# Optimization experiments

Hardware: AMD Instinct MI355X
Metric: run time of the kernel (lower is better)

## Reference

```python
import jax, jax.numpy as jnp
import numpy as np

N = 262144
DIM = 256
NUM_HEADS = 4
HEAD_DIM = DIM // NUM_HEADS
B = 4096
SCALE = HEAD_DIM ** (-0.5)
EPS = 1e-8


def setup_inputs() -> dict:
    key = jax.random.key(0)
    ks = jax.random.split(key, 7)
    x = jax.random.normal(ks[0], (N, DIM), dtype=jnp.float32)
    batch = jnp.sort(jax.random.randint(ks[1], (N,), 0, B)).astype(jnp.int64)
    query = jax.random.normal(ks[2], (NUM_HEADS, HEAD_DIM), dtype=jnp.float32)
    # nn.Linear default init scale ~ 1/sqrt(dim); keep exp() well-behaved
    key_w = jax.random.normal(ks[3], (DIM, DIM), dtype=jnp.float32) / np.sqrt(DIM)
    key_b = jax.random.normal(ks[4], (DIM,), dtype=jnp.float32) * 0.01
    value_w = jax.random.normal(ks[5], (DIM, DIM), dtype=jnp.float32) / np.sqrt(DIM)
    value_b = jax.random.normal(ks[6], (DIM,), dtype=jnp.float32) * 0.01
    return {"x": x, "batch": batch, "query": query, "key_w": key_w,
            "key_b": key_b, "value_w": value_w, "value_b": value_b}


def reference(x, batch, query, key_w, key_b, value_w, value_b):
    # k, v: [N, H, Hd]  (torch Linear: x @ W.T + b)
    k = (x @ key_w.T + key_b).reshape(N, NUM_HEADS, HEAD_DIM)
    v = (x @ value_w.T + value_b).reshape(N, NUM_HEADS, HEAD_DIM)
    # attn: [N, H] -- dot of learned per-head query with each node's key
    attn = jnp.einsum('hd,nhd->nh', query, k) * SCALE
    attn_exp = jnp.exp(attn)  # faithful: no max-subtraction in original
    # segment softmax denominator gathered back to nodes: [N, H]
    attn_sum = jax.ops.segment_sum(attn_exp, batch, num_segments=B)[batch]
    attn_norm = attn_exp / (attn_sum + EPS)
    # weighted values scatter-added per segment: [B, H, Hd]
    weighted = attn_norm[:, :, None] * v
    pooled = jax.ops.segment_sum(weighted, batch, num_segments=B)
    return pooled.reshape(B, DIM)
```

## Files before the change

kernel.cpp:

```cpp
#include <hip/hip_runtime.h>


constexpr int DIM = 256;
constexpr int NH  = 4;
constexpr int HD  = 64;
constexpr float SCL  = 0.125f;
constexpr float EPSV = 1e-8f;

constexpr int WS_QW   = 0;
constexpr int WS_QB   = 1024;
constexpr int WS_OFFS = 1088;
constexpr int WS_VWT  = 8192;
constexpr int WS_SRAW = 73728;

__global__ void prep_qw(const float* __restrict__ query,
                        const float* __restrict__ key_w,
                        const float* __restrict__ key_b,
                        float* __restrict__ ws){
  int t = blockIdx.x * 256 + threadIdx.x;
  int h = t >> 8, j = t & 255;
  float acc = 0.f;
  #pragma unroll 8
  for (int d = 0; d < HD; ++d)
    acc += query[h*HD+d] * key_w[(size_t)(h*HD+d)*DIM + j];
  ws[WS_QW + t] = acc;
  if (j == 0){
    float bb = 0.f;
    for (int d = 0; d < HD; ++d)
      bb += query[h*HD+d] * key_b[h*HD+d];
    ws[WS_QB + h] = bb;
  }
}

__global__ void prep_vwt(const float* __restrict__ value_w, float* __restrict__ ws){
  int jj = blockIdx.x;
  int t  = threadIdx.x;
  float4 v = *(const float4*)(value_w + (size_t)t*DIM + 4*jj);
  ((float4*)(ws + WS_VWT))[jj*256 + t] = v;
}

__global__ void seg_offsets(const int* __restrict__ batch32,
                            int* __restrict__ offs, int N, int B){
  int i = blockIdx.x * 256 + threadIdx.x;
  if (i >= N) return;
  const bool is64 = (batch32[N-1] == 0);
  int v  = is64 ? batch32[2*i] : batch32[i];
  int vp = (i == 0) ? -1 : (is64 ? batch32[2*(i-1)] : batch32[i-1]);
  for (int b = vp + 1; b <= v; ++b) offs[b] = i;
  if (i == N-1)
    for (int b = v + 1; b <= B; ++b) offs[b] = N;
}

__global__ __launch_bounds__(256, 4)
void attn_pool_split(const float* __restrict__ x,
                     const int* __restrict__ offs,
                     const float* __restrict__ ws,
                     float* __restrict__ sraw,
                     float* __restrict__ esum){
  __shared__ __align__(16) float S_all[4][NH*DIM];
  __shared__ float sums_all[4][NH];

  const int bid = blockIdx.x;
  const int b   = bid >> 1, part = bid & 1;
  const int tid = threadIdx.x;
  const int s = offs[b], e = offs[b+1];
  const int len = e - s;
  const int h1  = (len + 1) >> 1;
  const int ps  = s + part * h1;
  const int pe  = part ? e : (s + h1);

  const int wave = tid >> 6, lane = tid & 63;
  const int half = lane >> 5, sl = lane & 31;
  const int sigma = wave * 2 + half;

  float qwr[NH][8];
  #pragma unroll
  for (int h = 0; h < NH; ++h){
    float4 a = *(const float4*)(ws + WS_QW + h*DIM + 4*sl);
    float4 c = *(const float4*)(ws + WS_QW + h*DIM + 128 + 4*sl);
    qwr[h][0]=a.x; qwr[h][1]=a.y; qwr[h][2]=a.z; qwr[h][3]=a.w;
    qwr[h][4]=c.x; qwr[h][5]=c.y; qwr[h][6]=c.z; qwr[h][7]=c.w;
  }
  float qb[NH];
  #pragma unroll
  for (int h = 0; h < NH; ++h) qb[h] = ws[WS_QB + h];

  float Sacc[NH][8];
  #pragma unroll
  for (int h = 0; h < NH; ++h)
    #pragma unroll
    for (int c = 0; c < 8; ++c) Sacc[h][c] = 0.f;
  float se[NH] = {0.f, 0.f, 0.f, 0.f};

  const float4* xr4 = (const float4*)x;
  const float4 Z = make_float4(0.f, 0.f, 0.f, 0.f);

  int n0 = ps + sigma*2;
  bool v0 = n0 < pe;
  bool v1 = n0 + 1 < pe;
  float4 a0=Z, b0=Z, a1=Z, b1=Z;
  if (v0){ a0 = xr4[(size_t)n0*64 + sl];     b0 = xr4[(size_t)n0*64 + 32 + sl]; }
  if (v1){ a1 = xr4[(size_t)(n0+1)*64 + sl]; b1 = xr4[(size_t)(n0+1)*64 + 32 + sl]; }

  while (v0){
    const int nn = n0 + 16;
    const bool w0 = nn < pe;
    const bool w1 = nn + 1 < pe;
    float4 c0=Z, d0=Z, c1=Z, d1=Z;
    if (w0){ c0 = xr4[(size_t)nn*64 + sl];     d0 = xr4[(size_t)nn*64 + 32 + sl]; }
    if (w1){ c1 = xr4[(size_t)(nn+1)*64 + sl]; d1 = xr4[(size_t)(nn+1)*64 + 32 + sl]; }

    float xv0[8] = {a0.x,a0.y,a0.z,a0.w,b0.x,b0.y,b0.z,b0.w};
    float xv1[8] = {a1.x,a1.y,a1.z,a1.w,b1.x,b1.y,b1.z,b1.w};

    float p0[NH], p1[NH];
    #pragma unroll
    for (int h = 0; h < NH; ++h){
      float s0 = 0.f, s1 = 0.f;
      #pragma unroll
      for (int c = 0; c < 8; ++c){ s0 += qwr[h][c]*xv0[c]; s1 += qwr[h][c]*xv1[c]; }
      p0[h] = s0; p1[h] = s1;
    }
    #pragma unroll
    for (int m = 1; m < 32; m <<= 1){
      #pragma unroll
      for (int h = 0; h < NH; ++h){
        p0[h] += __shfl_xor(p0[h], m, 64);
        p1[h] += __shfl_xor(p1[h], m, 64);
      }
    }
    const float g1 = v1 ? 1.f : 0.f;
    #pragma unroll
    for (int h = 0; h < NH; ++h){
      float e0 = __expf((p0[h] + qb[h]) * SCL);
      float e1 = __expf((p1[h] + qb[h]) * SCL) * g1;
      se[h] += e0 + e1;
      #pragma unroll
      for (int c = 0; c < 8; ++c)
        Sacc[h][c] += e0*xv0[c] + e1*xv1[c];
    }
    n0 = nn; v0 = w0; v1 = w1;
    a0 = c0; b0 = d0; a1 = c1; b1 = d1;
  }

  #pragma unroll
  for (int h = 0; h < NH; ++h){
    se[h] += __shfl_xor(se[h], 32, 64);
    #pragma unroll
    for (int c = 0; c < 8; ++c) Sacc[h][c] += __shfl_xor(Sacc[h][c], 32, 64);
  }
  if (half == 0){
    #pragma unroll
    for (int h = 0; h < NH; ++h){
      float4 lo = make_float4(Sacc[h][0], Sacc[h][1], Sacc[h][2], Sacc[h][3]);
      float4 hi = make_float4(Sacc[h][4], Sacc[h][5], Sacc[h][6], Sacc[h][7]);
      *(float4*)&S_all[wave][h*DIM + 4*sl]       = lo;
      *(float4*)&S_all[wave][h*DIM + 128 + 4*sl] = hi;
    }
    if (sl == 0){
      #pragma unroll
      for (int h = 0; h < NH; ++h) sums_all[wave][h] = se[h];
    }
  }
  __syncthreads();

  #pragma unroll
  for (int k = 0; k < 4; ++k){
    const int idx = tid + k*256;
    float sv = 0.f;
    #pragma unroll
    for (int w = 0; w < 4; ++w) sv += S_all[w][idx];
    sraw[(size_t)bid*1024 + idx] = sv;
  }
  if (tid < NH){
    float tot = 0.f;
    #pragma unroll
    for (int w = 0; w < 4; ++w) tot += sums_all[w][tid];
    esum[bid*4 + tid] = tot;
  }
}

__global__ __launch_bounds__(256, 4)
void val_proj(const float* __restrict__ ws,
              const float* __restrict__ sraw,
              const float* __restrict__ esum,
              const float* __restrict__ value_b,
              float* __restrict__ out){
  constexpr int TB = 8;
  __shared__ __align__(16) float Sl[NH*DIM*TB];
  const int b0  = blockIdx.x * TB;
  const int tid = threadIdx.x;

  for (int idx = tid; idx < NH*DIM*TB; idx += 256){
    const int i = idx >> 10, rem = idx & 1023;
    const size_t base = (size_t)(b0 + i) * 2048;
    Sl[rem*TB + i] = sraw[base + rem] + sraw[base + 1024 + rem];
  }
  __syncthreads();

  const int t = tid, h = t >> 6;
  const float4* vwt4 = (const float4*)(ws + WS_VWT);
  float acc[TB];
  #pragma unroll
  for (int i = 0; i < TB; ++i) acc[i] = 0.f;

  #pragma unroll 4
  for (int jj = 0; jj < 64; ++jj){
    const float4 w4 = vwt4[jj*256 + t];
    #pragma unroll
    for (int r = 0; r < 4; ++r){
      const float* sp = &Sl[(h*256 + 4*jj + r)*TB];
      const float4 s0 = *(const float4*)sp;
      const float4 s1 = *(const float4*)(sp + 4);
      const float wr = (&w4.x)[r];
      acc[0] += wr*s0.x; acc[1] += wr*s0.y; acc[2] += wr*s0.z; acc[3] += wr*s0.w;
      acc[4] += wr*s1.x; acc[5] += wr*s1.y; acc[6] += wr*s1.z; acc[7] += wr*s1.w;
    }
  }
  const float vb = value_b[t];
  #pragma unroll
  for (int i = 0; i < TB; ++i){
    const float es  = esum[(b0 + i)*8 + h] + esum[(b0 + i)*8 + 4 + h];
    const float inv = 1.f / (es + EPSV);
    out[(size_t)(b0 + i)*256 + t] = acc[i]*inv + es*inv*vb;
  }
}

template<int MODE>
__global__ __launch_bounds__(512, 4)
void attn_pool_fused(const float* __restrict__ x,
                     const int* __restrict__ offs,
                     const float* __restrict__ ws,
                     const float* __restrict__ value_w,
                     const float* __restrict__ value_b,
                     float* __restrict__ out){
  constexpr int LDSF = (MODE == 1) ? (8192 + 32 + 1024 + 2048 + 8)
                                   : (8192 + 32 + 1024 + 512 + 8);
  __shared__ __align__(16) float lds[LDSF];
  float* S_all    = lds;
  float* sums_all = lds + 8192;

  const int b   = blockIdx.x;
  const int tid = threadIdx.x;
  const int seg_start = offs[b];
  const int seg_end   = offs[b+1];

  const int wave = tid >> 6, lane = tid & 63;
  const int half = lane >> 5, sl = lane & 31;
  const int sigma = wave * 2 + half;

  float qwr[NH][8];
  #pragma unroll
  for (int h = 0; h < NH; ++h){
    float4 a = *(const float4*)(ws + WS_QW + h*DIM + 4*sl);
    float4 c = *(const float4*)(ws + WS_QW + h*DIM + 128 + 4*sl);
    qwr[h][0]=a.x; qwr[h][1]=a.y; qwr[h][2]=a.z; qwr[h][3]=a.w;
    qwr[h][4]=c.x; qwr[h][5]=c.y; qwr[h][6]=c.z; qwr[h][7]=c.w;
  }
  float qb[NH];
  #pragma unroll
  for (int h = 0; h < NH; ++h) qb[h] = ws[WS_QB + h];

  float Sacc[NH][8];
  #pragma unroll
  for (int h = 0; h < NH; ++h)
    #pragma unroll
    for (int c = 0; c < 8; ++c) Sacc[h][c] = 0.f;
  float se[NH] = {0.f, 0.f, 0.f, 0.f};

  const float4* xr4 = (const float4*)x;
  const float4 Z = make_float4(0.f, 0.f, 0.f, 0.f);

  int n0 = seg_start + sigma*2;
  bool v0 = n0 < seg_end;
  bool v1 = n0 + 1 < seg_end;
  float4 a0=Z, b0=Z, a1=Z, b1=Z;
  if (v0){ a0 = xr4[(size_t)n0*64 + sl];     b0 = xr4[(size_t)n0*64 + 32 + sl]; }
  if (v1){ a1 = xr4[(size_t)(n0+1)*64 + sl]; b1 = xr4[(size_t)(n0+1)*64 + 32 + sl]; }

  while (v0){
    const int nn = n0 + 32;
    const bool w0 = nn < seg_end;
    const bool w1 = nn + 1 < seg_end;
    float4 c0=Z, d0=Z, c1=Z, d1=Z;
    if (w0){ c0 = xr4[(size_t)nn*64 + sl];     d0 = xr4[(size_t)nn*64 + 32 + sl]; }
    if (w1){ c1 = xr4[(size_t)(nn+1)*64 + sl]; d1 = xr4[(size_t)(nn+1)*64 + 32 + sl]; }

    float xv0[8] = {a0.x,a0.y,a0.z,a0.w,b0.x,b0.y,b0.z,b0.w};
    float xv1[8] = {a1.x,a1.y,a1.z,a1.w,b1.x,b1.y,b1.z,b1.w};

    float p0[NH], p1[NH];
    #pragma unroll
    for (int h = 0; h < NH; ++h){
      float s0 = 0.f, s1 = 0.f;
      #pragma unroll
      for (int c = 0; c < 8; ++c){ s0 += qwr[h][c]*xv0[c]; s1 += qwr[h][c]*xv1[c]; }
      p0[h] = s0; p1[h] = s1;
    }
    #pragma unroll
    for (int m = 1; m < 32; m <<= 1){
      #pragma unroll
      for (int h = 0; h < NH; ++h){
        p0[h] += __shfl_xor(p0[h], m, 64);
        p1[h] += __shfl_xor(p1[h], m, 64);
      }
    }
    const float g1 = v1 ? 1.f : 0.f;
    #pragma unroll
    for (int h = 0; h < NH; ++h){
      float e0 = __expf((p0[h] + qb[h]) * SCL);
      float e1 = __expf((p1[h] + qb[h]) * SCL) * g1;
      se[h] += e0 + e1;
      #pragma unroll
      for (int c = 0; c < 8; ++c)
        Sacc[h][c] += e0*xv0[c] + e1*xv1[c];
    }
    n0 = nn; v0 = w0; v1 = w1;
    a0 = c0; b0 = d0; a1 = c1; b1 = d1;
  }

  #pragma unroll
  for (int h = 0; h < NH; ++h){
    se[h] += __shfl_xor(se[h], 32, 64);
    #pragma unroll
    for (int c = 0; c < 8; ++c) Sacc[h][c] += __shfl_xor(Sacc[h][c], 32, 64);
  }
  if (half == 0){
    #pragma unroll
    for (int h = 0; h < NH; ++h){
      float4 lo = make_float4(Sacc[h][0], Sacc[h][1], Sacc[h][2], Sacc[h][3]);
      float4 hi = make_float4(Sacc[h][4], Sacc[h][5], Sacc[h][6], Sacc[h][7]);
      *(float4*)&S_all[wave*1024 + h*DIM + 4*sl]       = lo;
      *(float4*)&S_all[wave*1024 + h*DIM + 128 + 4*sl] = hi;
    }
    if (sl == 0){
      #pragma unroll
      for (int h = 0; h < NH; ++h) sums_all[wave*4 + h] = se[h];
    }
  }
  __syncthreads();

  float* Sfin  = lds + 8224;
  float* invs  = (MODE == 1) ? lds + 11296 : lds + 9760;
  float* wsums = invs + 4;
  #pragma unroll
  for (int k = 0; k < 2; ++k){
    const int idx = tid + k*512;
    float sv = 0.f;
    #pragma unroll
    for (int w = 0; w < 8; ++w) sv += S_all[w*1024 + idx];
    Sfin[idx] = sv;
  }
  if (tid < NH){
    float tot = 0.f;
    #pragma unroll
    for (int w = 0; w < 8; ++w) tot += sums_all[w*4 + tid];
    float inv = 1.f / (tot + EPSV);
    invs[tid] = inv; wsums[tid] = tot * inv;
  }
  __syncthreads();

  if constexpr (MODE == 1){
    float* ep = lds + 9248;
    const float4* vwt4 = (const float4*)(ws + WS_VWT);
    const int hh = lane >> 4;
    float4 acc = make_float4(0.f, 0.f, 0.f, 0.f);
    for (int jj = wave*8; jj < wave*8 + 8; ++jj){
      float4 q0 = vwt4[jj*256 + 4*lane + 0];
      float4 q1 = vwt4[jj*256 + 4*lane + 1];
      float4 q2 = vwt4[jj*256 + 4*lane + 2];
      float4 q3 = vwt4[jj*256 + 4*lane + 3];
      float4 sf = *(const float4*)&Sfin[hh*256 + 4*jj];
      acc.x += q0.x*sf.x + q0.y*sf.y + q0.z*sf.z + q0.w*sf.w;
      acc.y += q1.x*sf.x + q1.y*sf.y + q1.z*sf.z + q1.w*sf.w;
      acc.z += q2.x*sf.x + q2.y*sf.y + q2.z*sf.z + q2.w*sf.w;
      acc.w += q3.x*sf.x + q3.y*sf.y + q3.z*sf.z + q3.w*sf.w;
    }
    *(float4*)&ep[wave*256 + 4*lane] = acc;
    __syncthreads();
    if (tid < 256){
      const int t = tid, h2 = t >> 6;
      float sv = 0.f;
      #pragma unroll
      for (int w = 0; w < 8; ++w) sv += ep[w*256 + t];
      out[(size_t)b*256 + t] = sv * invs[h2] + wsums[h2] * value_b[t];
    }
  } else {
    float* ep2 = lds + 9248;
    const int t = tid & 255, part = tid >> 8;
    const int h2 = t >> 6;
    const float4* vrow = (const float4*)(value_w + (size_t)t * DIM) + part*32;
    const float4* sp   = (const float4*)&Sfin[h2*256] + part*32;
    float acc = 0.f;
    #pragma unroll
    for (int q = 0; q < 32; ++q){
      float4 r = vrow[q];
      float4 sv = sp[q];
      acc += r.x*sv.x + r.y*sv.y + r.z*sv.z + r.w*sv.w;
    }
    ep2[part*256 + t] = acc;
    __syncthreads();
    if (part == 0)
      out[(size_t)b * DIM + t] = (ep2[t] + ep2[256 + t]) * invs[h2] + wsums[h2] * value_b[t];
  }
}

extern "C" void kernel_launch(void* const* d_in, const int* in_sizes, int n_in,
                              void* d_out, int out_size, void* d_ws, size_t ws_size,
                              hipStream_t stream){
  const float* x       = (const float*)d_in[0];
  const int*   batch   = (const int*)d_in[1];
  const float* query   = (const float*)d_in[2];
  const float* key_w   = (const float*)d_in[3];
  const float* key_b   = (const float*)d_in[4];
  const float* value_w = (const float*)d_in[5];
  const float* value_b = (const float*)d_in[6];
  float* ws  = (float*)d_ws;
  float* out = (float*)d_out;

  const int N = in_sizes[1];
  const int B = out_size / DIM;

  int*   offs = (int*)(ws + WS_OFFS);
  float* sraw = ws + WS_SRAW;
  float* esum = ws + WS_SRAW + (size_t)B*2048;

  const size_t need_split = ((size_t)WS_SRAW + (size_t)B*2048 + (size_t)B*8) * sizeof(float);
  const size_t need_vwt   = ((size_t)WS_VWT + 65536) * sizeof(float);

  prep_qw<<<4, 256, 0, stream>>>(query, key_w, key_b, ws);
  seg_offsets<<<(N + 255) / 256, 256, 0, stream>>>(batch, offs, N, B);

  if (ws_size >= need_split){
    prep_vwt<<<64, 256, 0, stream>>>(value_w, ws);
    attn_pool_split<<<2*B, 256, 0, stream>>>(x, offs, ws, sraw, esum);
    val_proj<<<B / 8, 256, 0, stream>>>(ws, sraw, esum, value_b, out);
  } else if (ws_size >= need_vwt){
    prep_vwt<<<64, 256, 0, stream>>>(value_w, ws);
    attn_pool_fused<1><<<B, 512, 0, stream>>>(x, offs, ws, value_w, value_b, out);
  } else {
    attn_pool_fused<2><<<B, 512, 0, stream>>>(x, offs, ws, value_w, value_b, out);
  }
}
```

Before: 410.5 us.

## Use one block per segment with full-wave rows and padded LDS in projection

The attention pooling kernel now runs one block per segment instead of two half-segment blocks. Each wave covers a whole 256-float row per node (one float4 per lane) and processes four nodes per iteration with a full 64-lane reduction. This removes the second partial-sum buffer and the cross-block combine in the projection kernel, and halves the sraw traffic. The projection kernel pads its shared layout to stride 9, trading vector LDS loads for scalar loads to avoid bank conflicts. The cost is half as many blocks, so less parallelism on uneven segments, and more shuffle steps per node.

```diff
diff --git a/kernel.cpp b/kernel.cpp
--- a/kernel.cpp
+++ b/kernel.cpp
@@ -52,131 +52,112 @@
 }
 
 __global__ __launch_bounds__(256, 4)
-void attn_pool_split(const float* __restrict__ x,
-                     const int* __restrict__ offs,
-                     const float* __restrict__ ws,
-                     float* __restrict__ sraw,
-                     float* __restrict__ esum){
+void attn_pool3(const float* __restrict__ x,
+                const int* __restrict__ offs,
+                const float* __restrict__ ws,
+                float* __restrict__ sraw,
+                float* __restrict__ esum){
   __shared__ __align__(16) float S_all[4][NH*DIM];
   __shared__ float sums_all[4][NH];
 
-  const int bid = blockIdx.x;
-  const int b   = bid >> 1, part = bid & 1;
+  const int b   = blockIdx.x;
   const int tid = threadIdx.x;
   const int s = offs[b], e = offs[b+1];
-  const int len = e - s;
-  const int h1  = (len + 1) >> 1;
-  const int ps  = s + part * h1;
-  const int pe  = part ? e : (s + h1);
 
   const int wave = tid >> 6, lane = tid & 63;
-  const int half = lane >> 5, sl = lane & 31;
-  const int sigma = wave * 2 + half;
-
-  float qwr[NH][8];
+
+  float qwr[NH][4];
   #pragma unroll
   for (int h = 0; h < NH; ++h){
-    float4 a = *(const float4*)(ws + WS_QW + h*DIM + 4*sl);
-    float4 c = *(const float4*)(ws + WS_QW + h*DIM + 128 + 4*sl);
-    qwr[h][0]=a.x; qwr[h][1]=a.y; qwr[h][2]=a.z; qwr[h][3]=a.w;
-    qwr[h][4]=c.x; qwr[h][5]=c.y; qwr[h][6]=c.z; qwr[h][7]=c.w;
+    float4 q = *(const float4*)(ws + WS_QW + h*DIM + 4*lane);
+    qwr[h][0]=q.x; qwr[h][1]=q.y; qwr[h][2]=q.z; qwr[h][3]=q.w;
   }
   float qb[NH];
   #pragma unroll
   for (int h = 0; h < NH; ++h) qb[h] = ws[WS_QB + h];
 
-  float Sacc[NH][8];
+  float Sacc[NH][4];
   #pragma unroll
   for (int h = 0; h < NH; ++h)
     #pragma unroll
-    for (int c = 0; c < 8; ++c) Sacc[h][c] = 0.f;
+    for (int c = 0; c < 4; ++c) Sacc[h][c] = 0.f;
   float se[NH] = {0.f, 0.f, 0.f, 0.f};
 
   const float4* xr4 = (const float4*)x;
-  const float4 Z = make_float4(0.f, 0.f, 0.f, 0.f);
-
-  int n0 = ps + sigma*2;
-  bool v0 = n0 < pe;
-  bool v1 = n0 + 1 < pe;
-  float4 a0=Z, b0=Z, a1=Z, b1=Z;
-  if (v0){ a0 = xr4[(size_t)n0*64 + sl];     b0 = xr4[(size_t)n0*64 + 32 + sl]; }
-  if (v1){ a1 = xr4[(size_t)(n0+1)*64 + sl]; b1 = xr4[(size_t)(n0+1)*64 + 32 + sl]; }
-
-  while (v0){
+
+  int n0 = s + (wave << 2);
+  float4 A[4]; bool g[4];
+  #pragma unroll
+  for (int i = 0; i < 4; ++i){
+    g[i] = (n0 + i) < e;
+    const int safe = g[i] ? (n0 + i) : 0;
+    A[i] = xr4[(size_t)safe * 64 + lane];
+  }
+
+  while (n0 < e){
     const int nn = n0 + 16;
-    const bool w0 = nn < pe;
-    const bool w1 = nn + 1 < pe;
-    float4 c0=Z, d0=Z, c1=Z, d1=Z;
-    if (w0){ c0 = xr4[(size_t)nn*64 + sl];     d0 = xr4[(size_t)nn*64 + 32 + sl]; }
-    if (w1){ c1 = xr4[(size_t)(nn+1)*64 + sl]; d1 = xr4[(size_t)(nn+1)*64 + 32 + sl]; }
-
-    float xv0[8] = {a0.x,a0.y,a0.z,a0.w,b0.x,b0.y,b0.z,b0.w};
-    float xv1[8] = {a1.x,a1.y,a1.z,a1.w,b1.x,b1.y,b1.z,b1.w};
-
-    float p0[NH], p1[NH];
-    #pragma unroll
-    for (int h = 0; h < NH; ++h){
-      float s0 = 0.f, s1 = 0.f;
-      #pragma unroll
-      for (int c = 0; c < 8; ++c){ s0 += qwr[h][c]*xv0[c]; s1 += qwr[h][c]*xv1[c]; }
-      p0[h] = s0; p1[h] = s1;
-    }
-    #pragma unroll
-    for (int m = 1; m < 32; m <<= 1){
+    float4 An[4]; bool gn[4];
+    #pragma unroll
+    for (int i = 0; i < 4; ++i){
+      gn[i] = (nn + i) < e;
+      const int safe = gn[i] ? (nn + i) : 0;
+      An[i] = xr4[(size_t)safe * 64 + lane];
+    }
+
+    float p[4][NH];
+    #pragma unroll
+    for (int i = 0; i < 4; ++i)
+      #pragma unroll
+      for (int h = 0; h < NH; ++h)
+        p[i][h] = qwr[h][0]*A[i].x + qwr[h][1]*A[i].y
+                + qwr[h][2]*A[i].z + qwr[h][3]*A[i].w;
+
+    #pragma unroll
+    for (int m = 1; m < 64; m <<= 1){
+      #pragma unroll
+      for (int i = 0; i < 4; ++i)
+        #pragma unroll
+        for (int h = 0; h < NH; ++h)
+          p[i][h] += __shfl_xor(p[i][h], m, 64);
+    }
+
+    #pragma unroll
+    for (int i = 0; i < 4; ++i){
       #pragma unroll
       for (int h = 0; h < NH; ++h){
-        p0[h] += __shfl_xor(p0[h], m, 64);
-        p1[h] += __shfl_xor(p1[h], m, 64);
+        const float ev = g[i] ? __expf((p[i][h] + qb[h]) * SCL) : 0.f;
+        se[h] += ev;
+        Sacc[h][0] += ev * A[i].x;
+        Sacc[h][1] += ev * A[i].y;
+        Sacc[h][2] += ev * A[i].z;
+        Sacc[h][3] += ev * A[i].w;
       }
     }
-    const float g1 = v1 ? 1.f : 0.f;
-    #pragma unroll
-    for (int h = 0; h < NH; ++h){
-      float e0 = __expf((p0[h] + qb[h]) * SCL);
-      float e1 = __expf((p1[h] + qb[h]) * SCL) * g1;
-      se[h] += e0 + e1;
-      #pragma unroll
-      for (int c = 0; c < 8; ++c)
-        Sacc[h][c] += e0*xv0[c] + e1*xv1[c];
-    }
-    n0 = nn; v0 = w0; v1 = w1;
-    a0 = c0; b0 = d0; a1 = c1; b1 = d1;
-  }
-
-  #pragma unroll
-  for (int h = 0; h < NH; ++h){
-    se[h] += __shfl_xor(se[h], 32, 64);
-    #pragma unroll
-    for (int c = 0; c < 8; ++c) Sacc[h][c] += __shfl_xor(Sacc[h][c], 32, 64);
-  }
-  if (half == 0){
-    #pragma unroll
-    for (int h = 0; h < NH; ++h){
-      float4 lo = make_float4(Sacc[h][0], Sacc[h][1], Sacc[h][2], Sacc[h][3]);
-      float4 hi = make_float4(Sacc[h][4], Sacc[h][5], Sacc[h][6], Sacc[h][7]);
-      *(float4*)&S_all[wave][h*DIM + 4*sl]       = lo;
-      *(float4*)&S_all[wave][h*DIM + 128 + 4*sl] = hi;
-    }
-    if (sl == 0){
-      #pragma unroll
-      for (int h = 0; h < NH; ++h) sums_all[wave][h] = se[h];
-    }
+
+    n0 = nn;
+    #pragma unroll
+    for (int i = 0; i < 4; ++i){ A[i] = An[i]; g[i] = gn[i]; }
+  }
+
+  #pragma unroll
+  for (int h = 0; h < NH; ++h)
+    *(float4*)&S_all[wave][h*DIM + 4*lane] =
+        make_float4(Sacc[h][0], Sacc[h][1], Sacc[h][2], Sacc[h][3]);
+  if (lane == 0){
+    #pragma unroll
+    for (int h = 0; h < NH; ++h) sums_all[wave][h] = se[h];
   }
   __syncthreads();
 
   #pragma unroll
   for (int k = 0; k < 4; ++k){
     const int idx = tid + k*256;
-    float sv = 0.f;
-    #pragma unroll
-    for (int w = 0; w < 4; ++w) sv += S_all[w][idx];
-    sraw[(size_t)bid*1024 + idx] = sv;
+    const float sv = S_all[0][idx] + S_all[1][idx] + S_all[2][idx] + S_all[3][idx];
+    sraw[(size_t)b*1024 + idx] = sv;
   }
   if (tid < NH){
-    float tot = 0.f;
-    #pragma unroll
-    for (int w = 0; w < 4; ++w) tot += sums_all[w][tid];
-    esum[bid*4 + tid] = tot;
+    esum[b*4 + tid] = sums_all[0][tid] + sums_all[1][tid]
+                    + sums_all[2][tid] + sums_all[3][tid];
   }
 }
 
@@ -186,15 +167,15 @@
               const float* __restrict__ esum,
               const float* __restrict__ value_b,
               float* __restrict__ out){
-  constexpr int TB = 8;
-  __shared__ __align__(16) float Sl[NH*DIM*TB];
+  constexpr int TB  = 8;
+  constexpr int TBP = 9;
+  __shared__ __align__(16) float Sl[NH*DIM*TBP];
   const int b0  = blockIdx.x * TB;
   const int tid = threadIdx.x;
 
   for (int idx = tid; idx < NH*DIM*TB; idx += 256){
     const int i = idx >> 10, rem = idx & 1023;
-    const size_t base = (size_t)(b0 + i) * 2048;
-    Sl[rem*TB + i] = sraw[base + rem] + sraw[base + 1024 + rem];
+    Sl[rem*TBP + i] = sraw[(size_t)(b0 + i)*1024 + rem];
   }
   __syncthreads();
 
@@ -209,18 +190,16 @@
     const float4 w4 = vwt4[jj*256 + t];
     #pragma unroll
     for (int r = 0; r < 4; ++r){
-      const float* sp = &Sl[(h*256 + 4*jj + r)*TB];
-      const float4 s0 = *(const float4*)sp;
-      const float4 s1 = *(const float4*)(sp + 4);
+      const float* sp = &Sl[(h*256 + 4*jj + r)*TBP];
       const float wr = (&w4.x)[r];
-      acc[0] += wr*s0.x; acc[1] += wr*s0.y; acc[2] += wr*s0.z; acc[3] += wr*s0.w;
-      acc[4] += wr*s1.x; acc[5] += wr*s1.y; acc[6] += wr*s1.z; acc[7] += wr*s1.w;
+      acc[0] += wr*sp[0]; acc[1] += wr*sp[1]; acc[2] += wr*sp[2]; acc[3] += wr*sp[3];
+      acc[4] += wr*sp[4]; acc[5] += wr*sp[5]; acc[6] += wr*sp[6]; acc[7] += wr*sp[7];
     }
   }
   const float vb = value_b[t];
   #pragma unroll
   for (int i = 0; i < TB; ++i){
-    const float es  = esum[(b0 + i)*8 + h] + esum[(b0 + i)*8 + 4 + h];
+    const float es  = esum[(b0 + i)*4 + h];
     const float inv = 1.f / (es + EPSV);
     out[(size_t)(b0 + i)*256 + t] = acc[i]*inv + es*inv*vb;
   }
@@ -269,7 +248,7 @@
   float se[NH] = {0.f, 0.f, 0.f, 0.f};
 
   const float4* xr4 = (const float4*)x;
-  const float4 Z = make_float4(0.f, 0.f, 0.f, 0.f);
+  const float4 Z = make_float4(0.f,0.f,0.f,0.f);
 
   int n0 = seg_start + sigma*2;
   bool v0 = n0 < seg_end;
@@ -423,9 +402,9 @@
 
   int*   offs = (int*)(ws + WS_OFFS);
   float* sraw = ws + WS_SRAW;
-  float* esum = ws + WS_SRAW + (size_t)B*2048;
-
-  const size_t need_split = ((size_t)WS_SRAW + (size_t)B*2048 + (size_t)B*8) * sizeof(float);
+  float* esum = ws + WS_SRAW + (size_t)B*1024;
+
+  const size_t need_split = ((size_t)WS_SRAW + (size_t)B*1024 + (size_t)B*4) * sizeof(float);
   const size_t need_vwt   = ((size_t)WS_VWT + 65536) * sizeof(float);
 
   prep_qw<<<4, 256, 0, stream>>>(query, key_w, key_b, ws);
@@ -433,7 +412,7 @@
 
   if (ws_size >= need_split){
     prep_vwt<<<64, 256, 0, stream>>>(value_w, ws);
-    attn_pool_split<<<2*B, 256, 0, stream>>>(x, offs, ws, sraw, esum);
+    attn_pool3<<<B, 256, 0, stream>>>(x, offs, ws, sraw, esum);
     val_proj<<<B / 8, 256, 0, stream>>>(ws, sraw, esum, value_b, out);
   } else if (ws_size >= need_vwt){
     prep_vwt<<<64, 256, 0, stream>>>(value_w, ws);
```

Result: no change. 418.0 us (+1.8%).

## Fuse segment pooling with value projection, merge prep kernels, use DPP reductions

Applied to the files above, without the earlier changes.

Merges the three preparation kernels (query-key fold, value weight transpose, segment offsets) into one launch. It replaces the split-segment pooling plus separate value projection kernel with a single per-segment kernel that reduces in LDS and applies the value projection directly, removing the intermediate sraw/esum round trip through global memory and one launch. The per-row dot-product reduction now uses DPP row rotates plus a ds_swizzle instead of shfl_xor. In exchange each segment is handled by one 256-thread block instead of two, which halves parallelism on the streaming phase, and value_w rows are re-read per segment instead of being reused across 8 segments.

```diff
diff --git a/kernel.cpp b/kernel.cpp
--- a/kernel.cpp
+++ b/kernel.cpp
@@ -11,63 +11,75 @@
 constexpr int WS_QB   = 1024;
 constexpr int WS_OFFS = 1088;
 constexpr int WS_VWT  = 8192;
-constexpr int WS_SRAW = 73728;
-
-__global__ void prep_qw(const float* __restrict__ query,
-                        const float* __restrict__ key_w,
-                        const float* __restrict__ key_b,
-                        float* __restrict__ ws){
-  int t = blockIdx.x * 256 + threadIdx.x;
-  int h = t >> 8, j = t & 255;
-  float acc = 0.f;
-  #pragma unroll 8
-  for (int d = 0; d < HD; ++d)
-    acc += query[h*HD+d] * key_w[(size_t)(h*HD+d)*DIM + j];
-  ws[WS_QW + t] = acc;
-  if (j == 0){
-    float bb = 0.f;
+
+template<int CTRL>
+__device__ __forceinline__ float dpp_ror_add(float v){
+  int r = __builtin_amdgcn_update_dpp(0, __float_as_int(v), CTRL, 0xF, 0xF, false);
+  return v + __int_as_float(r);
+}
+__device__ __forceinline__ float red32(float v){
+  v = dpp_ror_add<0x121>(v);
+  v = dpp_ror_add<0x122>(v);
+  v = dpp_ror_add<0x124>(v);
+  v = dpp_ror_add<0x128>(v);
+  int r = __builtin_amdgcn_ds_swizzle(__float_as_int(v), 0x401F);
+  return v + __int_as_float(r);
+}
+
+__global__ void prep_seg(const float* __restrict__ query,
+                         const float* __restrict__ key_w,
+                         const float* __restrict__ key_b,
+                         const float* __restrict__ value_w,
+                         const int* __restrict__ batch32,
+                         float* __restrict__ ws,
+                         int* __restrict__ offs,
+                         int N, int B, int do_vwt){
+  const int bid = blockIdx.x, tid = threadIdx.x;
+  if (bid < 64){
+    if (do_vwt){
+      float4 v = *(const float4*)(value_w + (size_t)tid*DIM + 4*bid);
+      ((float4*)(ws + WS_VWT))[bid*256 + tid] = v;
+    }
+  } else if (bid < 68){
+    int t = (bid - 64)*256 + tid;
+    int h = t >> 8, j = t & 255;
+    float acc = 0.f;
+    #pragma unroll 8
     for (int d = 0; d < HD; ++d)
-      bb += query[h*HD+d] * key_b[h*HD+d];
-    ws[WS_QB + h] = bb;
-  }
-}
-
-__global__ void prep_vwt(const float* __restrict__ value_w, float* __restrict__ ws){
-  int jj = blockIdx.x;
-  int t  = threadIdx.x;
-  float4 v = *(const float4*)(value_w + (size_t)t*DIM + 4*jj);
-  ((float4*)(ws + WS_VWT))[jj*256 + t] = v;
-}
-
-__global__ void seg_offsets(const int* __restrict__ batch32,
-                            int* __restrict__ offs, int N, int B){
-  int i = blockIdx.x * 256 + threadIdx.x;
-  if (i >= N) return;
-  const bool is64 = (batch32[N-1] == 0);
-  int v  = is64 ? batch32[2*i] : batch32[i];
-  int vp = (i == 0) ? -1 : (is64 ? batch32[2*(i-1)] : batch32[i-1]);
-  for (int b = vp + 1; b <= v; ++b) offs[b] = i;
-  if (i == N-1)
-    for (int b = v + 1; b <= B; ++b) offs[b] = N;
+      acc += query[h*HD+d] * key_w[(size_t)(h*HD+d)*DIM + j];
+    ws[WS_QW + t] = acc;
+    if (j == 0){
+      float bb = 0.f;
+      for (int d = 0; d < HD; ++d)
+        bb += query[h*HD+d] * key_b[h*HD+d];
+      ws[WS_QB + h] = bb;
+    }
+  } else {
+    int i = (bid - 68)*256 + tid;
+    if (i >= N) return;
+    const bool is64 = (batch32[N-1] == 0);
+    int v  = is64 ? batch32[2*i] : batch32[i];
+    int vp = (i == 0) ? -1 : (is64 ? batch32[2*(i-1)] : batch32[i-1]);
+    for (int b = vp + 1; b <= v; ++b) offs[b] = i;
+    if (i == N-1)
+      for (int b = v + 1; b <= B; ++b) offs[b] = N;
+  }
 }
 
 __global__ __launch_bounds__(256, 4)
-void attn_pool_split(const float* __restrict__ x,
-                     const int* __restrict__ offs,
-                     const float* __restrict__ ws,
-                     float* __restrict__ sraw,
-                     float* __restrict__ esum){
+void attn_fused2(const float* __restrict__ x,
+                 const int* __restrict__ offs,
+                 const float* __restrict__ ws,
+                 const float* __restrict__ value_b,
+                 float* __restrict__ out){
   __shared__ __align__(16) float S_all[4][NH*DIM];
+  __shared__ __align__(16) float Sfin[NH*DIM];
   __shared__ float sums_all[4][NH];
-
-  const int bid = blockIdx.x;
-  const int b   = bid >> 1, part = bid & 1;
+  __shared__ float invs[NH], wsums[NH];
+
+  const int b   = blockIdx.x;
   const int tid = threadIdx.x;
   const int s = offs[b], e = offs[b+1];
-  const int len = e - s;
-  const int h1  = (len + 1) >> 1;
-  const int ps  = s + part * h1;
-  const int pe  = part ? e : (s + h1);
 
   const int wave = tid >> 6, lane = tid & 63;
   const int half = lane >> 5, sl = lane & 31;
@@ -95,17 +107,17 @@
   const float4* xr4 = (const float4*)x;
   const float4 Z = make_float4(0.f, 0.f, 0.f, 0.f);
 
-  int n0 = ps + sigma*2;
-  bool v0 = n0 < pe;
-  bool v1 = n0 + 1 < pe;
+  int n0 = s + sigma*2;
+  bool v0 = n0 < e;
+  bool v1 = n0 + 1 < e;
   float4 a0=Z, b0=Z, a1=Z, b1=Z;
   if (v0){ a0 = xr4[(size_t)n0*64 + sl];     b0 = xr4[(size_t)n0*64 + 32 + sl]; }
   if (v1){ a1 = xr4[(size_t)(n0+1)*64 + sl]; b1 = xr4[(size_t)(n0+1)*64 + 32 + sl]; }
 
   while (v0){
     const int nn = n0 + 16;
-    const bool w0 = nn < pe;
-    const bool w1 = nn + 1 < pe;
+    const bool w0 = nn < e;
+    const bool w1 = nn + 1 < e;
     float4 c0=Z, d0=Z, c1=Z, d1=Z;
     if (w0){ c0 = xr4[(size_t)nn*64 + sl];     d0 = xr4[(size_t)nn*64 + 32 + sl]; }
     if (w1){ c1 = xr4[(size_t)(nn+1)*64 + sl]; d1 = xr4[(size_t)(nn+1)*64 + 32 + sl]; }
@@ -122,12 +134,9 @@
       p0[h] = s0; p1[h] = s1;
     }
     #pragma unroll
-    for (int m = 1; m < 32; m <<= 1){
-      #pragma unroll
-      for (int h = 0; h < NH; ++h){
-        p0[h] += __shfl_xor(p0[h], m, 64);
-        p1[h] += __shfl_xor(p1[h], m, 64);
-      }
+    for (int h = 0; h < NH; ++h){
+      p0[h] = red32(p0[h]);
+      p1[h] = red32(p1[h]);
     }
     const float g1 = v1 ? 1.f : 0.f;
     #pragma unroll
@@ -167,66 +176,30 @@
   #pragma unroll
   for (int k = 0; k < 4; ++k){
     const int idx = tid + k*256;
-    float sv = 0.f;
-    #pragma unroll
-    for (int w = 0; w < 4; ++w) sv += S_all[w][idx];
-    sraw[(size_t)bid*1024 + idx] = sv;
+    Sfin[idx] = S_all[0][idx] + S_all[1][idx] + S_all[2][idx] + S_all[3][idx];
   }
   if (tid < NH){
-    float tot = 0.f;
-    #pragma unroll
-    for (int w = 0; w < 4; ++w) tot += sums_all[w][tid];
-    esum[bid*4 + tid] = tot;
-  }
-}
-
-__global__ __launch_bounds__(256, 4)
-void val_proj(const float* __restrict__ ws,
-              const float* __restrict__ sraw,
-              const float* __restrict__ esum,
-              const float* __restrict__ value_b,
-              float* __restrict__ out){
-  constexpr int TB = 8;
-  __shared__ __align__(16) float Sl[NH*DIM*TB];
-  const int b0  = blockIdx.x * TB;
-  const int tid = threadIdx.x;
-
-  for (int idx = tid; idx < NH*DIM*TB; idx += 256){
-    const int i = idx >> 10, rem = idx & 1023;
-    const size_t base = (size_t)(b0 + i) * 2048;
-    Sl[rem*TB + i] = sraw[base + rem] + sraw[base + 1024 + rem];
+    float tot = sums_all[0][tid] + sums_all[1][tid]
+              + sums_all[2][tid] + sums_all[3][tid];
+    float inv = 1.f / (tot + EPSV);
+    invs[tid]  = inv;
+    wsums[tid] = tot * inv;
   }
   __syncthreads();
 
   const int t = tid, h = t >> 6;
   const float4* vwt4 = (const float4*)(ws + WS_VWT);
-  float acc[TB];
-  #pragma unroll
-  for (int i = 0; i < TB; ++i) acc[i] = 0.f;
-
-  #pragma unroll 4
+  const float4* sp   = (const float4*)&Sfin[h*256];
+  float acc = 0.f;
+  #pragma unroll 8
   for (int jj = 0; jj < 64; ++jj){
     const float4 w4 = vwt4[jj*256 + t];
-    #pragma unroll
-    for (int r = 0; r < 4; ++r){
-      const float* sp = &Sl[(h*256 + 4*jj + r)*TB];
-      const float4 s0 = *(const float4*)sp;
-      const float4 s1 = *(const float4*)(sp + 4);
-      const float wr = (&w4.x)[r];
-      acc[0] += wr*s0.x; acc[1] += wr*s0.y; acc[2] += wr*s0.z; acc[3] += wr*s0.w;
-      acc[4] += wr*s1.x; acc[5] += wr*s1.y; acc[6] += wr*s1.z; acc[7] += wr*s1.w;
-    }
-  }
-  const float vb = value_b[t];
-  #pragma unroll
-  for (int i = 0; i < TB; ++i){
-    const float es  = esum[(b0 + i)*8 + h] + esum[(b0 + i)*8 + 4 + h];
-    const float inv = 1.f / (es + EPSV);
-    out[(size_t)(b0 + i)*256 + t] = acc[i]*inv + es*inv*vb;
-  }
-}
-
-template<int MODE>
+    const float4 s4 = sp[jj];
+    acc += w4.x*s4.x + w4.y*s4.y + w4.z*s4.z + w4.w*s4.w;
+  }
+  out[(size_t)b*256 + t] = acc * invs[h] + wsums[h] * value_b[t];
+}
+
 __global__ __launch_bounds__(512, 4)
 void attn_pool_fused(const float* __restrict__ x,
                      const int* __restrict__ offs,
@@ -234,9 +207,7 @@
                      const float* __restrict__ value_w,
                      const float* __restrict__ value_b,
                      float* __restrict__ out){
-  constexpr int LDSF = (MODE == 1) ? (8192 + 32 + 1024 + 2048 + 8)
-                                   : (8192 + 32 + 1024 + 512 + 8);
-  __shared__ __align__(16) float lds[LDSF];
+  __shared__ __align__(16) float lds[8192 + 32 + 1024 + 512 + 8];
   float* S_all    = lds;
   float* sums_all = lds + 8192;
 
@@ -269,7 +240,7 @@
   float se[NH] = {0.f, 0.f, 0.f, 0.f};
 
   const float4* xr4 = (const float4*)x;
-  const float4 Z = make_float4(0.f, 0.f, 0.f, 0.f);
+  const float4 Z = make_float4(0.f,0.f,0.f,0.f);
 
   int n0 = seg_start + sigma*2;
   bool v0 = n0 < seg_end;
@@ -341,7 +312,7 @@
   __syncthreads();
 
   float* Sfin  = lds + 8224;
-  float* invs  = (MODE == 1) ? lds + 11296 : lds + 9760;
+  float* invs  = lds + 9760;
   float* wsums = invs + 4;
   #pragma unroll
   for (int k = 0; k < 2; ++k){
@@ -360,49 +331,22 @@
   }
   __syncthreads();
 
-  if constexpr (MODE == 1){
-    float* ep = lds + 9248;
-    const float4* vwt4 = (const float4*)(ws + WS_VWT);
-    const int hh = lane >> 4;
-    float4 acc = make_float4(0.f, 0.f, 0.f, 0.f);
-    for (int jj = wave*8; jj < wave*8 + 8; ++jj){
-      float4 q0 = vwt4[jj*256 + 4*lane + 0];
-      float4 q1 = vwt4[jj*256 + 4*lane + 1];
-      float4 q2 = vwt4[jj*256 + 4*lane + 2];
-      float4 q3 = vwt4[jj*256 + 4*lane + 3];
-      float4 sf = *(const float4*)&Sfin[hh*256 + 4*jj];
-      acc.x += q0.x*sf.x + q0.y*sf.y + q0.z*sf.z + q0.w*sf.w;
-      acc.y += q1.x*sf.x + q1.y*sf.y + q1.z*sf.z + q1.w*sf.w;
-      acc.z += q2.x*sf.x + q2.y*sf.y + q2.z*sf.z + q2.w*sf.w;
-      acc.w += q3.x*sf.x + q3.y*sf.y + q3.z*sf.z + q3.w*sf.w;
-    }
-    *(float4*)&ep[wave*256 + 4*lane] = acc;
-    __syncthreads();
-    if (tid < 256){
-      const int t = tid, h2 = t >> 6;
-      float sv = 0.f;
-      #pragma unroll
-      for (int w = 0; w < 8; ++w) sv += ep[w*256 + t];
-      out[(size_t)b*256 + t] = sv * invs[h2] + wsums[h2] * value_b[t];
-    }
-  } else {
-    float* ep2 = lds + 9248;
-    const int t = tid & 255, part = tid >> 8;
-    const int h2 = t >> 6;
-    const float4* vrow = (const float4*)(value_w + (size_t)t * DIM) + part*32;
-    const float4* sp   = (const float4*)&Sfin[h2*256] + part*32;
-    float acc = 0.f;
-    #pragma unroll
-    for (int q = 0; q < 32; ++q){
-      float4 r = vrow[q];
-      float4 sv = sp[q];
-      acc += r.x*sv.x + r.y*sv.y + r.z*sv.z + r.w*sv.w;
-    }
-    ep2[part*256 + t] = acc;
-    __syncthreads();
-    if (part == 0)
-      out[(size_t)b * DIM + t] = (ep2[t] + ep2[256 + t]) * invs[h2] + wsums[h2] * value_b[t];
-  }
+  float* ep2 = lds + 9248;
+  const int t = tid & 255, part = tid >> 8;
+  const int h2 = t >> 6;
+  const float4* vrow = (const float4*)(value_w + (size_t)t * DIM) + part*32;
+  const float4* sp   = (const float4*)&Sfin[h2*256] + part*32;
+  float acc = 0.f;
+  #pragma unroll
+  for (int q = 0; q < 32; ++q){
+    float4 r = vrow[q];
+    float4 sv = sp[q];
+    acc += r.x*sv.x + r.y*sv.y + r.z*sv.z + r.w*sv.w;
+  }
+  ep2[part*256 + t] = acc;
+  __syncthreads();
+  if (part == 0)
+    out[(size_t)b * DIM + t] = (ep2[t] + ep2[256 + t]) * invs[h2] + wsums[h2] * value_b[t];
 }
 
 extern "C" void kernel_launch(void* const* d_in, const int* in_sizes, int n_in,
@@ -421,24 +365,16 @@
   const int N = in_sizes[1];
   const int B = out_size / DIM;
 
-  int*   offs = (int*)(ws + WS_OFFS);
-  float* sraw = ws + WS_SRAW;
-  float* esum = ws + WS_SRAW + (size_t)B*2048;
-
-  const size_t need_split = ((size_t)WS_SRAW + (size_t)B*2048 + (size_t)B*8) * sizeof(float);
-  const size_t need_vwt   = ((size_t)WS_VWT + 65536) * sizeof(float);
-
-  prep_qw<<<4, 256, 0, stream>>>(query, key_w, key_b, ws);
-  seg_offsets<<<(N + 255) / 256, 256, 0, stream>>>(batch, offs, N, B);
-
-  if (ws_size >= need_split){
-    prep_vwt<<<64, 256, 0, stream>>>(value_w, ws);
-    attn_pool_split<<<2*B, 256, 0, stream>>>(x, offs, ws, sraw, esum);
-    val_proj<<<B / 8, 256, 0, stream>>>(ws, sraw, esum, value_b, out);
-  } else if (ws_size >= need_vwt){
-    prep_vwt<<<64, 256, 0, stream>>>(value_w, ws);
-    attn_pool_fused<1><<<B, 512, 0, stream>>>(x, offs, ws, value_w, value_b, out);
-  } else {
-    attn_pool_fused<2><<<B, 512, 0, stream>>>(x, offs, ws, value_w, value_b, out);
-  }
-}
+  int* offs = (int*)(ws + WS_OFFS);
+
+  const size_t need_vwt = ((size_t)WS_VWT + 65536) * sizeof(float);
+  const int do_vwt = (ws_size >= need_vwt) ? 1 : 0;
+
+  const int seg_blocks = (N + 255) / 256;
+  prep_seg<<<68 + seg_blocks, 256, 0, stream>>>(query, key_w, key_b, value_w,
+                                                batch, ws, offs, N, B, do_vwt);
+  if (do_vwt)
+    attn_fused2<<<B, 256, 0, stream>>>(x, offs, ws, value_b, out);
+  else
+    attn_pool_fused<<<B, 512, 0, stream>>>(x, offs, ws, value_w, value_b, out);
+}
```

Measured after the change: 393.4 us (median of 2 runs). 1.04x faster.
